# Kernel tuning notes

Hardware: AMD Instinct MI355X
Metric: run time of the kernel (lower is better)

The kernel has to match this reference:

```python
import jax, jax.numpy as jnp
import numpy as np

N, E = 50000, 800000
IN_DIM, HID, ZDIM = 256, 128, 64
LN_EPS = 1e-5


def _layernorm(x, gamma, beta):
    mu = jnp.mean(x, axis=-1, keepdims=True)
    var = jnp.mean(jnp.square(x - mu), axis=-1, keepdims=True)
    return (x - mu) * jax.lax.rsqrt(var + LN_EPS) * gamma + beta


def _gcn_conv(h, src, dst, dinv, W, b):
    # h: (N, d_in) -> (N, d_out). GCNConv: X W, then sym-normalized
    # aggregation over edges with self-loops, then bias.
    h = h @ W                                   # (N, d_out)
    coef = dinv[src] * dinv[dst]                # (E,)
    agg = jax.ops.segment_sum(h[src] * coef[:, None], dst,
                              num_segments=h.shape[0])
    agg = agg + h * jnp.square(dinv)[:, None]   # self-loop term
    return agg + b


def setup_inputs() -> dict:
    key = jax.random.key(0)
    ks = jax.random.split(key, 5)
    x = jax.random.normal(ks[0], (N, IN_DIM), dtype=jnp.float32)
    edge_index = jax.random.randint(ks[1], (2, E), 0, N, dtype=jnp.int64)
    s1 = 1.0 / np.sqrt(IN_DIM)
    s2 = 1.0 / np.sqrt(HID)
    return {
        "x": x,
        "edge_index": edge_index,
        "ln_gamma": jnp.ones((IN_DIM,), jnp.float32),
        "ln_beta": jnp.zeros((IN_DIM,), jnp.float32),
        "W1": jax.random.normal(ks[2], (IN_DIM, HID), jnp.float32) * s1,
        "b1": jnp.zeros((HID,), jnp.float32),
        "W2": jax.random.normal(ks[3], (HID, HID), jnp.float32) * s2,
        "b2": jnp.zeros((HID,), jnp.float32),
        "W3": jax.random.normal(ks[4], (HID, ZDIM), jnp.float32) * s2,
        "b3": jnp.zeros((ZDIM,), jnp.float32),
    }


def reference(x, edge_index, ln_gamma, ln_beta, W1, b1, W2, b2, W3, b3):
    src, dst = edge_index[0], edge_index[1]
    n = x.shape[0]
    # degree with self-loops (dropout is inference no-op, training=False)
    deg = jnp.ones((n,), x.dtype).at[dst].add(1.0)
    dinv = jax.lax.rsqrt(deg)
    h = _layernorm(x, ln_gamma, ln_beta)
    h = jax.nn.relu(_gcn_conv(h, src, dst, dinv, W1, b1))
    h = jax.nn.relu(_gcn_conv(h, src, dst, dinv, W2, b2))
    z = _gcn_conv(h, src, dst, dinv, W3, b3)
    return z
```

## Files before the change

kernel.cpp:

```cpp
#include <hip/hip_runtime.h>
#include <cstdint>
#include <cstddef>


typedef __attribute__((ext_vector_type(8))) __bf16 bf16x8;
typedef __attribute__((ext_vector_type(4))) float f32x4;
typedef _Float16 half_t;
typedef __attribute__((ext_vector_type(8))) _Float16 half8_t;

__global__ __launch_bounds__(256) void prep_misc(
    const float* __restrict__ x, const float* __restrict__ W1,
    const float* __restrict__ W2, const float* __restrict__ W3,
    int* __restrict__ bcnt, int* __restrict__ bcur_zero,
    unsigned short* __restrict__ W1t_hi, unsigned short* __restrict__ W1t_lo,
    unsigned short* __restrict__ W2t_hi, unsigned short* __restrict__ W2t_lo,
    unsigned short* __restrict__ W3t_hi, unsigned short* __restrict__ W3t_lo,
    float* __restrict__ mu, float* __restrict__ rs, int n) {
  int blk = blockIdx.x;
  int tid = threadIdx.x;
  if (blk == 0) {
    bcnt[tid] = 0;
    bcur_zero[tid] = 0;
    return;
  }
  if (blk <= 224) {
    int idx = (blk - 1) * 256 + tid;
    const float* W;
    unsigned short *Th, *Tl;
    int K, NOUT;
    if (idx < 32768) {
      W = W1; Th = W1t_hi; Tl = W1t_lo; K = 256; NOUT = 128;
    } else if (idx < 49152) {
      idx -= 32768;
      W = W2; Th = W2t_hi; Tl = W2t_lo; K = 128; NOUT = 128;
    } else {
      idx -= 49152;
      W = W3; Th = W3t_hi; Tl = W3t_lo; K = 128; NOUT = 64;
    }
    int k = idx / NOUT, c = idx % NOUT;
    float v = W[idx];
    __bf16 h = (__bf16)v;
    __bf16 l = (__bf16)(v - (float)h);
    Th[(size_t)c * K + k] = __builtin_bit_cast(unsigned short, h);
    Tl[(size_t)c * K + k] = __builtin_bit_cast(unsigned short, l);
    return;
  }
  int wv = (blk - 225) * 4 + (tid >> 6);
  int lane = tid & 63;
  if (wv >= n) return;
  const float4* row = (const float4*)(x + (size_t)wv * 256);
  float4 v = row[lane];
  float s = v.x + v.y + v.z + v.w;
  float s2 = v.x * v.x + v.y * v.y + v.z * v.z + v.w * v.w;
  for (int off = 32; off > 0; off >>= 1) {
    s += __shfl_down(s, off);
    s2 += __shfl_down(s2, off);
  }
  if (lane == 0) {
    float m = s * (1.0f / 256.0f);
    float var = s2 * (1.0f / 256.0f) - m * m;
    mu[wv] = m;
    rs[wv] = rsqrtf(var + 1e-5f);
  }
}

__global__ __launch_bounds__(256) void hist_bucket(const int* __restrict__ dst,
                                                   int* __restrict__ bcnt, int E, int NB) {
  __shared__ int h[256];
  int t = threadIdx.x;
  h[t] = 0;
  __syncthreads();
  for (int e = blockIdx.x * 256 + t; e < E; e += gridDim.x * 256)
    atomicAdd(&h[dst[e] >> 8], 1);
  __syncthreads();
  if (t < NB && h[t]) atomicAdd(&bcnt[t], h[t]);
}

__global__ __launch_bounds__(256) void scan_buckets(const int* __restrict__ bcnt,
                                                    int* __restrict__ bbase,
                                                    int* __restrict__ bcur, int NB, int E) {
  __shared__ int tmp[256];
  int t = threadIdx.x;
  int v = (t < NB) ? bcnt[t] : 0;
  tmp[t] = v;
  __syncthreads();
  for (int off = 1; off < 256; off <<= 1) {
    int x = (t >= off) ? tmp[t - off] : 0;
    __syncthreads();
    tmp[t] += x;
    __syncthreads();
  }
  int excl = tmp[t] - v;
  if (t < NB) { bbase[t] = excl; bcur[t] = excl; }
  if (t == 0) bbase[NB] = E;
}

#define CHUNK 4096
__global__ __launch_bounds__(256) void scatter_bins(const int* __restrict__ src,
                                                    const int* __restrict__ dst,
                                                    int* __restrict__ bcur,
                                                    int2* __restrict__ binned, int E) {
  __shared__ int2 recs[CHUNK];
  __shared__ int hist[256], lbase[256], resv[256], cur[256];
  int t = threadIdx.x;
  int e0 = blockIdx.x * CHUNK;
  if (e0 >= E) return;
  int len = min(CHUNK, E - e0);
  hist[t] = 0;
  cur[t] = 0;
  __syncthreads();
  for (int i = t; i < len; i += 256) atomicAdd(&hist[dst[e0 + i] >> 8], 1);
  __syncthreads();
  int v = hist[t];
  lbase[t] = v;
  __syncthreads();
  for (int off = 1; off < 256; off <<= 1) {
    int x = (t >= off) ? lbase[t - off] : 0;
    __syncthreads();
    lbase[t] += x;
    __syncthreads();
  }
  int myexcl = lbase[t] - v;
  if (v) resv[t] = atomicAdd(&bcur[t], v);
  __syncthreads();
  lbase[t] = myexcl;
  __syncthreads();
  for (int i = t; i < len; i += 256) {
    int d = dst[e0 + i], s = src[e0 + i];
    int b = d >> 8;
    int r = atomicAdd(&cur[b], 1);
    recs[lbase[b] + r] = make_int2(s, d);
  }
  __syncthreads();
  for (int i = t; i < len; i += 256) {
    int2 rc = recs[i];
    int b = rc.y >> 8;
    binned[resv[b] + (i - lbase[b])] = rc;
  }
}

#define MAXB 8192
__global__ __launch_bounds__(256) void sort_bucket(const int2* __restrict__ binned,
                                                   const int* __restrict__ bbase,
                                                   int* __restrict__ srcs,
                                                   int* __restrict__ offs,
                                                   float* __restrict__ dinv,
                                                   int N, int NB, int E) {
  __shared__ int2 recs[MAXB];
  __shared__ unsigned short rnk[MAXB];
  __shared__ int sstage[MAXB];
  __shared__ int hist[256], nbase[256];
  int b = blockIdx.x, t = threadIdx.x;
  int base = bbase[b], end = bbase[b + 1];
  int L = end - base;
  if (L > MAXB) L = MAXB;
  hist[t] = 0;
  __syncthreads();
  for (int i = t; i < L; i += 256) {
    int2 rc = binned[base + i];
    recs[i] = rc;
    int r = atomicAdd(&hist[rc.y & 255], 1);
    rnk[i] = (unsigned short)r;
  }
  __syncthreads();
  int v = hist[t];
  nbase[t] = v;
  __syncthreads();
  for (int off = 1; off < 256; off <<= 1) {
    int x = (t >= off) ? nbase[t - off] : 0;
    __syncthreads();
    nbase[t] += x;
    __syncthreads();
  }
  int excl = nbase[t] - v;
  __syncthreads();
  nbase[t] = excl;
  int node = (b << 8) + t;
  if (node < N) {
    offs[node] = base + excl;
    dinv[node] = rsqrtf(1.0f + (float)v);
  }
  if (b == NB - 1 && t == 0) offs[N] = E;
  __syncthreads();
  for (int i = t; i < L; i += 256) {
    int2 rc = recs[i];
    sstage[nbase[rc.y & 255] + rnk[i]] = rc.x;
  }
  __syncthreads();
  for (int i = t; i < L; i += 256) srcs[base + i] = sstage[i];
}

__global__ void fill_w(const int* __restrict__ srcs, const float* __restrict__ dinv,
                       int2* __restrict__ edges, int E) {
  int e = blockIdx.x * 256 + threadIdx.x;
  if (e < E) {
    int s = srcs[e];
    edges[e] = make_int2(s, __float_as_int(dinv[s]));
  }
}

template <int K, int NOUT, bool LN, bool A_FP16>
__launch_bounds__(256)
__global__ void gemm_mfma(const void* __restrict__ Avoid,
                          const unsigned short* __restrict__ Wt_hi,
                          const unsigned short* __restrict__ Wt_lo,
                          const float* __restrict__ mu, const float* __restrict__ rs,
                          const float* __restrict__ gamma, const float* __restrict__ beta,
                          half_t* __restrict__ out, int nrows) {
  constexpr int BM = 64, BK = 32;
  constexpr int NT = NOUT / 16;
  __shared__ unsigned short As_hi[BM][BK];
  __shared__ unsigned short As_lo[BM][BK];
  __shared__ unsigned short Bs_hi[NOUT][BK];
  __shared__ unsigned short Bs_lo[NOUT][BK];

  const int tid = threadIdx.x;
  const int lane = tid & 63;
  const int w = tid >> 6;
  const int quad = lane >> 4;
  const int l16 = lane & 15;
  const int row0 = blockIdx.x * BM;

  f32x4 acc[NT];
#pragma unroll
  for (int t = 0; t < NT; ++t) acc[t] = (f32x4){0.f, 0.f, 0.f, 0.f};

  for (int k0 = 0; k0 < K; k0 += BK) {
    if (!A_FP16) {
      const float* A = (const float*)Avoid;
#pragma unroll
      for (int i = 0; i < 2; ++i) {
        int r = i * 32 + (tid >> 3);
        int c4 = (tid & 7) * 4;
        int grow = row0 + r;
        if (grow > nrows - 1) grow = nrows - 1;
        float4 v = *(const float4*)&A[(size_t)grow * K + k0 + c4];
        if (LN) {
          float m = mu[grow], s = rs[grow];
          float4 g = *(const float4*)&gamma[k0 + c4];
          float4 b = *(const float4*)&beta[k0 + c4];
          v.x = (v.x - m) * s * g.x + b.x;
          v.y = (v.y - m) * s * g.y + b.y;
          v.z = (v.z - m) * s * g.z + b.z;
          v.w = (v.w - m) * s * g.w + b.w;
        }
        float vv[4] = {v.x, v.y, v.z, v.w};
#pragma unroll
        for (int j = 0; j < 4; ++j) {
          __bf16 h = (__bf16)vv[j];
          __bf16 l = (__bf16)(vv[j] - (float)h);
          As_hi[r][c4 + j] = __builtin_bit_cast(unsigned short, h);
          As_lo[r][c4 + j] = __builtin_bit_cast(unsigned short, l);
        }
      }
    } else {
      const half_t* A = (const half_t*)Avoid;
      int r = tid >> 2;
      int c8 = (tid & 3) * 8;
      int grow = row0 + r;
      if (grow > nrows - 1) grow = nrows - 1;
      half8_t v = *(const half8_t*)&A[(size_t)grow * K + k0 + c8];
#pragma unroll
      for (int j = 0; j < 8; ++j) {
        float f = (float)v[j];
        __bf16 h = (__bf16)f;
        __bf16 l = (__bf16)(f - (float)h);
        As_hi[r][c8 + j] = __builtin_bit_cast(unsigned short, h);
        As_lo[r][c8 + j] = __builtin_bit_cast(unsigned short, l);
      }
    }
#pragma unroll
    for (int i = 0; i < NOUT / 64; ++i) {
      int n = i * 64 + (tid >> 2);
      int c8 = (tid & 3) * 8;
      *(uint4*)&Bs_hi[n][c8] = *(const uint4*)&Wt_hi[(size_t)n * K + k0 + c8];
      *(uint4*)&Bs_lo[n][c8] = *(const uint4*)&Wt_lo[(size_t)n * K + k0 + c8];
    }
    __syncthreads();

    bf16x8 ah = *(const bf16x8*)&As_hi[w * 16 + l16][quad * 8];
    bf16x8 al = *(const bf16x8*)&As_lo[w * 16 + l16][quad * 8];
#pragma unroll
    for (int t = 0; t < NT; ++t) {
      bf16x8 bh = *(const bf16x8*)&Bs_hi[t * 16 + l16][quad * 8];
      bf16x8 bl = *(const bf16x8*)&Bs_lo[t * 16 + l16][quad * 8];
      acc[t] = __builtin_amdgcn_mfma_f32_16x16x32_bf16(ah, bh, acc[t], 0, 0, 0);
      acc[t] = __builtin_amdgcn_mfma_f32_16x16x32_bf16(al, bh, acc[t], 0, 0, 0);
      acc[t] = __builtin_amdgcn_mfma_f32_16x16x32_bf16(ah, bl, acc[t], 0, 0, 0);
    }
    __syncthreads();
  }

#pragma unroll
  for (int t = 0; t < NT; ++t) {
#pragma unroll
    for (int r = 0; r < 4; ++r) {
      int grow = row0 + w * 16 + quad * 4 + r;
      if (grow < nrows) out[(size_t)grow * NOUT + t * 16 + l16] = (half_t)acc[t][r];
    }
  }
}

__global__ __launch_bounds__(256) void agg128_h(const half_t* __restrict__ t,
                                                const int* __restrict__ offs,
                                                const int2* __restrict__ edges,
                                                const float* __restrict__ dinv,
                                                const float* __restrict__ bias,
                                                half_t* __restrict__ out, int n) {
  int gid = blockIdx.x * blockDim.x + threadIdx.x;
  int node = gid >> 6, lane = gid & 63;
  if (node >= n) return;
  int qw = lane >> 4;
  int fl = lane & 15;
  int e0 = offs[node], e1 = offs[node + 1];
  float acc[8] = {0.f, 0.f, 0.f, 0.f, 0.f, 0.f, 0.f, 0.f};
  int e = e0 + qw;
  for (; e + 12 < e1; e += 16) {
    int2 da = edges[e], db = edges[e + 4], dc = edges[e + 8], dd = edges[e + 12];
    half8_t va = *(const half8_t*)(t + ((size_t)da.x << 7) + fl * 8);
    half8_t vb = *(const half8_t*)(t + ((size_t)db.x << 7) + fl * 8);
    half8_t vc = *(const half8_t*)(t + ((size_t)dc.x << 7) + fl * 8);
    half8_t vd = *(const half8_t*)(t + ((size_t)dd.x << 7) + fl * 8);
    float wa = __int_as_float(da.y), wb = __int_as_float(db.y);
    float wc = __int_as_float(dc.y), wd = __int_as_float(dd.y);
#pragma unroll
    for (int j = 0; j < 8; ++j) {
      acc[j] = fmaf(wa, (float)va[j], acc[j]);
      acc[j] = fmaf(wb, (float)vb[j], acc[j]);
      acc[j] = fmaf(wc, (float)vc[j], acc[j]);
      acc[j] = fmaf(wd, (float)vd[j], acc[j]);
    }
  }
  for (; e < e1; e += 4) {
    int2 d = edges[e];
    half8_t v = *(const half8_t*)(t + ((size_t)d.x << 7) + fl * 8);
    float w = __int_as_float(d.y);
#pragma unroll
    for (int j = 0; j < 8; ++j) acc[j] = fmaf(w, (float)v[j], acc[j]);
  }
#pragma unroll
  for (int j = 0; j < 8; ++j) {
    acc[j] += __shfl_xor(acc[j], 16);
    acc[j] += __shfl_xor(acc[j], 32);
  }
  if (qw == 0) {
    float di = dinv[node];
    float dii = di * di;
    half8_t sv = *(const half8_t*)(t + ((size_t)node << 7) + fl * 8);
    float4 b0 = *(const float4*)(bias + fl * 8);
    float4 b1 = *(const float4*)(bias + fl * 8 + 4);
    float bb[8] = {b0.x, b0.y, b0.z, b0.w, b1.x, b1.y, b1.z, b1.w};
    half8_t o;
#pragma unroll
    for (int j = 0; j < 8; ++j) {
      float v = di * acc[j] + dii * (float)sv[j] + bb[j];
      o[j] = (half_t)fmaxf(v, 0.f);
    }
    *(half8_t*)(out + ((size_t)node << 7) + fl * 8) = o;
  }
}

__global__ __launch_bounds__(256) void agg64_h(const half_t* __restrict__ t,
                                               const int* __restrict__ offs,
                                               const int2* __restrict__ edges,
                                               const float* __restrict__ dinv,
                                               const float* __restrict__ bias,
                                               float* __restrict__ out, int n) {
  int gid = blockIdx.x * blockDim.x + threadIdx.x;
  int node = gid >> 6, lane = gid & 63;
  if (node >= n) return;
  int og = lane >> 3;
  int fl = lane & 7;
  int e0 = offs[node], e1 = offs[node + 1];
  float acc[8] = {0.f, 0.f, 0.f, 0.f, 0.f, 0.f, 0.f, 0.f};
  int e = e0 + og;
  for (; e + 8 < e1; e += 16) {
    int2 da = edges[e], db = edges[e + 8];
    half8_t va = *(const half8_t*)(t + ((size_t)da.x << 6) + fl * 8);
    half8_t vb = *(const half8_t*)(t + ((size_t)db.x << 6) + fl * 8);
    float wa = __int_as_float(da.y), wb = __int_as_float(db.y);
#pragma unroll
    for (int j = 0; j < 8; ++j) {
      acc[j] = fmaf(wa, (float)va[j], acc[j]);
      acc[j] = fmaf(wb, (float)vb[j], acc[j]);
    }
  }
  for (; e < e1; e += 8) {
    int2 d = edges[e];
    half8_t v = *(const half8_t*)(t + ((size_t)d.x << 6) + fl * 8);
    float w = __int_as_float(d.y);
#pragma unroll
    for (int j = 0; j < 8; ++j) acc[j] = fmaf(w, (float)v[j], acc[j]);
  }
#pragma unroll
  for (int j = 0; j < 8; ++j) {
    acc[j] += __shfl_xor(acc[j], 8);
    acc[j] += __shfl_xor(acc[j], 16);
    acc[j] += __shfl_xor(acc[j], 32);
  }
  if (og == 0) {
    float di = dinv[node];
    float dii = di * di;
    half8_t sv = *(const half8_t*)(t + ((size_t)node << 6) + fl * 8);
    float4 b0 = *(const float4*)(bias + fl * 8);
    float4 b1 = *(const float4*)(bias + fl * 8 + 4);
    float bb[8] = {b0.x, b0.y, b0.z, b0.w, b1.x, b1.y, b1.z, b1.w};
    float ov[8];
#pragma unroll
    for (int j = 0; j < 8; ++j) ov[j] = di * acc[j] + dii * (float)sv[j] + bb[j];
    *(float4*)(out + ((size_t)node << 6) + fl * 8) = make_float4(ov[0], ov[1], ov[2], ov[3]);
    *(float4*)(out + ((size_t)node << 6) + fl * 8 + 4) = make_float4(ov[4], ov[5], ov[6], ov[7]);
  }
}

extern "C" void kernel_launch(void* const* d_in, const int* in_sizes, int n_in,
                              void* d_out, int out_size, void* d_ws, size_t ws_size,
                              hipStream_t stream) {
  const float* x = (const float*)d_in[0];
  const int* ei = (const int*)d_in[1];
  const float* gamma = (const float*)d_in[2];
  const float* beta = (const float*)d_in[3];
  const float* W1 = (const float*)d_in[4];
  const float* b1 = (const float*)d_in[5];
  const float* W2 = (const float*)d_in[6];
  const float* b2 = (const float*)d_in[7];
  const float* W3 = (const float*)d_in[8];
  const float* b3 = (const float*)d_in[9];
  float* out = (float*)d_out;

  const int N = in_sizes[0] / 256;
  const int E = in_sizes[1] / 2;
  const int* src = ei;
  const int* dst = ei + E;
  const int NB = (N + 255) >> 8;

  char* ws = (char*)d_ws;
  auto alloc = [&](size_t bytes) -> char* {
    char* p = ws;
    ws += (bytes + 255) & ~(size_t)255;
    return p;
  };
  int* bcnt = (int*)alloc(256 * 4);
  int* bbase = (int*)alloc(257 * 4);
  int* bcur = (int*)alloc(256 * 4);
  int2* binned = (int2*)alloc((size_t)E * 8);
  int* srcs = (int*)alloc((size_t)E * 4);
  int* offs = (int*)alloc((size_t)(N + 1) * 4);
  float* dinv = (float*)alloc((size_t)N * 4);
  int2* edges = (int2*)alloc((size_t)E * 8);
  float* mu = (float*)alloc((size_t)N * 4);
  float* rs = (float*)alloc((size_t)N * 4);
  half_t* t = (half_t*)alloc((size_t)N * 128 * 2);
  half_t* h = (half_t*)alloc((size_t)N * 128 * 2);
  unsigned short* W1t_hi = (unsigned short*)alloc(256 * 128 * 2);
  unsigned short* W1t_lo = (unsigned short*)alloc(256 * 128 * 2);
  unsigned short* W2t_hi = (unsigned short*)alloc(128 * 128 * 2);
  unsigned short* W2t_lo = (unsigned short*)alloc(128 * 128 * 2);
  unsigned short* W3t_hi = (unsigned short*)alloc(128 * 64 * 2);
  unsigned short* W3t_lo = (unsigned short*)alloc(128 * 64 * 2);

  const int ln_blocks = (N + 3) / 4;
  prep_misc<<<225 + ln_blocks, 256, 0, stream>>>(
      x, W1, W2, W3, bcnt, bcur, W1t_hi, W1t_lo, W2t_hi, W2t_lo, W3t_hi, W3t_lo,
      mu, rs, N);

  hist_bucket<<<256, 256, 0, stream>>>(dst, bcnt, E, NB);
  scan_buckets<<<1, 256, 0, stream>>>(bcnt, bbase, bcur, NB, E);
  scatter_bins<<<(E + CHUNK - 1) / CHUNK, 256, 0, stream>>>(src, dst, bcur, binned, E);
  sort_bucket<<<NB, 256, 0, stream>>>(binned, bbase, srcs, offs, dinv, N, NB, E);
  fill_w<<<(E + 255) / 256, 256, 0, stream>>>(srcs, dinv, edges, E);

  const int gemm_blocks = (N + 63) / 64;
  const int agg_blocks = (N + 3) / 4;

  gemm_mfma<256, 128, true, false><<<gemm_blocks, 256, 0, stream>>>(
      x, W1t_hi, W1t_lo, mu, rs, gamma, beta, t, N);
  agg128_h<<<agg_blocks, 256, 0, stream>>>(t, offs, edges, dinv, b1, h, N);

  gemm_mfma<128, 128, false, true><<<gemm_blocks, 256, 0, stream>>>(
      h, W2t_hi, W2t_lo, nullptr, nullptr, nullptr, nullptr, t, N);
  agg128_h<<<agg_blocks, 256, 0, stream>>>(t, offs, edges, dinv, b2, h, N);

  gemm_mfma<128, 64, false, true><<<gemm_blocks, 256, 0, stream>>>(
      h, W3t_hi, W3t_lo, nullptr, nullptr, nullptr, nullptr, t, N);
  agg64_h<<<agg_blocks, 256, 0, stream>>>(t, offs, edges, dinv, b3, out, N);
}
```

Before: 291.5 us.

## Double-buffer GEMM tiles via register prefetch and pack edge records into 32 bits

The MFMA GEMM now keeps two LDS buffers and prefetches the next K tile into registers while the current tile's MFMAs run. This needs only one barrier per iteration and hides part of the global-load latency. Edge binning now packs each (dst, src) pair into one 32-bit word, which halves binned traffic. The sort pass re-reads the packed words from global memory and assigns slots with shared-memory atomics instead of staging records and ranks in LDS. The packing assumes node ids fit in 16 bits, which holds for N=50000 but not in general, and atomic slot assignment makes the per-node edge order nondeterministic.

Result: slower. 317.9 us (+9.1%).

```diff
diff --git a/kernel.cpp b/kernel.cpp
--- a/kernel.cpp
+++ b/kernel.cpp
@@ -99,8 +99,8 @@
 __global__ __launch_bounds__(256) void scatter_bins(const int* __restrict__ src,
                                                     const int* __restrict__ dst,
                                                     int* __restrict__ bcur,
-                                                    int2* __restrict__ binned, int E) {
-  __shared__ int2 recs[CHUNK];
+                                                    unsigned int* __restrict__ binned, int E) {
+  __shared__ unsigned int recs[CHUNK];
   __shared__ int hist[256], lbase[256], resv[256], cur[256];
   int t = threadIdx.x;
   int e0 = blockIdx.x * CHUNK;
@@ -129,52 +129,46 @@
     int d = dst[e0 + i], s = src[e0 + i];
     int b = d >> 8;
     int r = atomicAdd(&cur[b], 1);
-    recs[lbase[b] + r] = make_int2(s, d);
+    recs[lbase[b] + r] = ((unsigned int)d << 16) | (unsigned int)s;
   }
   __syncthreads();
   for (int i = t; i < len; i += 256) {
-    int2 rc = recs[i];
-    int b = rc.y >> 8;
+    unsigned int rc = recs[i];
+    int b = rc >> 24;
     binned[resv[b] + (i - lbase[b])] = rc;
   }
 }
 
 #define MAXB 8192
-__global__ __launch_bounds__(256) void sort_bucket(const int2* __restrict__ binned,
+__global__ __launch_bounds__(256) void sort_bucket(const unsigned int* __restrict__ binned,
                                                    const int* __restrict__ bbase,
                                                    int* __restrict__ srcs,
                                                    int* __restrict__ offs,
                                                    float* __restrict__ dinv,
                                                    int N, int NB, int E) {
-  __shared__ int2 recs[MAXB];
-  __shared__ unsigned short rnk[MAXB];
   __shared__ int sstage[MAXB];
-  __shared__ int hist[256], nbase[256];
+  __shared__ int hist[256], nbase[256], cur[256], tmp[256];
   int b = blockIdx.x, t = threadIdx.x;
   int base = bbase[b], end = bbase[b + 1];
   int L = end - base;
   if (L > MAXB) L = MAXB;
   hist[t] = 0;
   __syncthreads();
-  for (int i = t; i < L; i += 256) {
-    int2 rc = binned[base + i];
-    recs[i] = rc;
-    int r = atomicAdd(&hist[rc.y & 255], 1);
-    rnk[i] = (unsigned short)r;
-  }
+  for (int i = t; i < L; i += 256)
+    atomicAdd(&hist[(binned[base + i] >> 16) & 255], 1);
   __syncthreads();
   int v = hist[t];
-  nbase[t] = v;
+  tmp[t] = v;
   __syncthreads();
   for (int off = 1; off < 256; off <<= 1) {
-    int x = (t >= off) ? nbase[t - off] : 0;
+    int x = (t >= off) ? tmp[t - off] : 0;
     __syncthreads();
-    nbase[t] += x;
+    tmp[t] += x;
     __syncthreads();
   }
-  int excl = nbase[t] - v;
-  __syncthreads();
+  int excl = tmp[t] - v;
   nbase[t] = excl;
+  cur[t] = excl;
   int node = (b << 8) + t;
   if (node < N) {
     offs[node] = base + excl;
@@ -183,8 +177,10 @@
   if (b == NB - 1 && t == 0) offs[N] = E;
   __syncthreads();
   for (int i = t; i < L; i += 256) {
-    int2 rc = recs[i];
-    sstage[nbase[rc.y & 255] + rnk[i]] = rc.x;
+    unsigned int p = binned[base + i];
+    int ld = (p >> 16) & 255;
+    int slot = atomicAdd(&cur[ld], 1);
+    sstage[slot] = (int)(p & 0xFFFFu);
   }
   __syncthreads();
   for (int i = t; i < L; i += 256) srcs[base + i] = sstage[i];
@@ -209,10 +205,12 @@
                           half_t* __restrict__ out, int nrows) {
   constexpr int BM = 64, BK = 32;
   constexpr int NT = NOUT / 16;
-  __shared__ unsigned short As_hi[BM][BK];
-  __shared__ unsigned short As_lo[BM][BK];
-  __shared__ unsigned short Bs_hi[NOUT][BK];
-  __shared__ unsigned short Bs_lo[NOUT][BK];
+  constexpr int T = K / BK;
+  constexpr int NBI = NOUT / 64;
+  __shared__ unsigned short As_hi[2][BM][BK];
+  __shared__ unsigned short As_lo[2][BM][BK];
+  __shared__ unsigned short Bs_hi[2][NOUT][BK];
+  __shared__ unsigned short Bs_lo[2][NOUT][BK];
 
   const int tid = threadIdx.x;
   const int lane = tid & 63;
@@ -221,74 +219,104 @@
   const int l16 = lane & 15;
   const int row0 = blockIdx.x * BM;
 
-  f32x4 acc[NT];
-#pragma unroll
-  for (int t = 0; t < NT; ++t) acc[t] = (f32x4){0.f, 0.f, 0.f, 0.f};
-
-  for (int k0 = 0; k0 < K; k0 += BK) {
+  float4 a0, a1, gv, bv;
+  half8_t av;
+  uint4 bhr[NBI], blr[NBI];
+  const int rA0 = tid >> 3, c4 = (tid & 7) * 4;
+  const int rA = tid >> 2, c8a = (tid & 3) * 8;
+  const int nB = tid >> 2, c8 = (tid & 3) * 8;
+  int g0 = row0 + rA0; if (g0 > nrows - 1) g0 = nrows - 1;
+  int g1 = row0 + 32 + rA0; if (g1 > nrows - 1) g1 = nrows - 1;
+  int gA = row0 + rA; if (gA > nrows - 1) gA = nrows - 1;
+  float m0 = 0.f, s0 = 0.f, m1 = 0.f, s1 = 0.f;
+  if (LN && !A_FP16) { m0 = mu[g0]; s0 = rs[g0]; m1 = mu[g1]; s1 = rs[g1]; }
+
+  auto load_tile = [&](int k0) {
     if (!A_FP16) {
       const float* A = (const float*)Avoid;
-#pragma unroll
-      for (int i = 0; i < 2; ++i) {
-        int r = i * 32 + (tid >> 3);
-        int c4 = (tid & 7) * 4;
-        int grow = row0 + r;
-        if (grow > nrows - 1) grow = nrows - 1;
-        float4 v = *(const float4*)&A[(size_t)grow * K + k0 + c4];
-        if (LN) {
-          float m = mu[grow], s = rs[grow];
-          float4 g = *(const float4*)&gamma[k0 + c4];
-          float4 b = *(const float4*)&beta[k0 + c4];
-          v.x = (v.x - m) * s * g.x + b.x;
-          v.y = (v.y - m) * s * g.y + b.y;
-          v.z = (v.z - m) * s * g.z + b.z;
-          v.w = (v.w - m) * s * g.w + b.w;
-        }
-        float vv[4] = {v.x, v.y, v.z, v.w};
-#pragma unroll
-        for (int j = 0; j < 4; ++j) {
-          __bf16 h = (__bf16)vv[j];
-          __bf16 l = (__bf16)(vv[j] - (float)h);
-          As_hi[r][c4 + j] = __builtin_bit_cast(unsigned short, h);
-          As_lo[r][c4 + j] = __builtin_bit_cast(unsigned short, l);
-        }
+      a0 = *(const float4*)&A[(size_t)g0 * K + k0 + c4];
+      a1 = *(const float4*)&A[(size_t)g1 * K + k0 + c4];
+      if (LN) {
+        gv = *(const float4*)&gamma[k0 + c4];
+        bv = *(const float4*)&beta[k0 + c4];
       }
     } else {
       const half_t* A = (const half_t*)Avoid;
-      int r = tid >> 2;
-      int c8 = (tid & 3) * 8;
-      int grow = row0 + r;
-      if (grow > nrows - 1) grow = nrows - 1;
-      half8_t v = *(const half8_t*)&A[(size_t)grow * K + k0 + c8];
+      av = *(const half8_t*)&A[(size_t)gA * K + k0 + c8a];
+    }
+#pragma unroll
+    for (int i = 0; i < NBI; ++i) {
+      int n = i * 64 + nB;
+      bhr[i] = *(const uint4*)&Wt_hi[(size_t)n * K + k0 + c8];
+      blr[i] = *(const uint4*)&Wt_lo[(size_t)n * K + k0 + c8];
+    }
+  };
+  auto store_tile = [&](int buf) {
+    if (!A_FP16) {
+      float v0[4] = {a0.x, a0.y, a0.z, a0.w};
+      float v1[4] = {a1.x, a1.y, a1.z, a1.w};
+      if (LN) {
+        float g4[4] = {gv.x, gv.y, gv.z, gv.w};
+        float b4[4] = {bv.x, bv.y, bv.z, bv.w};
+#pragma unroll
+        for (int j = 0; j < 4; ++j) {
+          v0[j] = (v0[j] - m0) * s0 * g4[j] + b4[j];
+          v1[j] = (v1[j] - m1) * s1 * g4[j] + b4[j];
+        }
+      }
+#pragma unroll
+      for (int j = 0; j < 4; ++j) {
+        __bf16 h0 = (__bf16)v0[j];
+        As_hi[buf][rA0][c4 + j] = __builtin_bit_cast(unsigned short, h0);
+        __bf16 l0 = (__bf16)(v0[j] - (float)h0);
+        As_lo[buf][rA0][c4 + j] = __builtin_bit_cast(unsigned short, l0);
+        __bf16 h1 = (__bf16)v1[j];
+        As_hi[buf][32 + rA0][c4 + j] = __builtin_bit_cast(unsigned short, h1);
+        __bf16 l1 = (__bf16)(v1[j] - (float)h1);
+        As_lo[buf][32 + rA0][c4 + j] = __builtin_bit_cast(unsigned short, l1);
+      }
+    } else {
 #pragma unroll
       for (int j = 0; j < 8; ++j) {
-        float f = (float)v[j];
+        float f = (float)av[j];
         __bf16 h = (__bf16)f;
         __bf16 l = (__bf16)(f - (float)h);
-        As_hi[r][c8 + j] = __builtin_bit_cast(unsigned short, h);
-        As_lo[r][c8 + j] = __builtin_bit_cast(unsigned short, l);
+        As_hi[buf][rA][c8a + j] = __builtin_bit_cast(unsigned short, h);
+        As_lo[buf][rA][c8a + j] = __builtin_bit_cast(unsigned short, l);
       }
     }
 #pragma unroll
-    for (int i = 0; i < NOUT / 64; ++i) {
-      int n = i * 64 + (tid >> 2);
-      int c8 = (tid & 3) * 8;
-      *(uint4*)&Bs_hi[n][c8] = *(const uint4*)&Wt_hi[(size_t)n * K + k0 + c8];
-      *(uint4*)&Bs_lo[n][c8] = *(const uint4*)&Wt_lo[(size_t)n * K + k0 + c8];
-    }
-    __syncthreads();
-
-    bf16x8 ah = *(const bf16x8*)&As_hi[w * 16 + l16][quad * 8];
-    bf16x8 al = *(const bf16x8*)&As_lo[w * 16 + l16][quad * 8];
+    for (int i = 0; i < NBI; ++i) {
+      int n = i * 64 + nB;
+      *(uint4*)&Bs_hi[buf][n][c8] = bhr[i];
+      *(uint4*)&Bs_lo[buf][n][c8] = blr[i];
+    }
+  };
+
+  f32x4 acc[NT];
+#pragma unroll
+  for (int t = 0; t < NT; ++t) acc[t] = (f32x4){0.f, 0.f, 0.f, 0.f};
+
+  load_tile(0);
+  store_tile(0);
+  __syncthreads();
+  for (int it = 0; it < T; ++it) {
+    const int cur = it & 1;
+    if (it + 1 < T) load_tile((it + 1) * BK);
+    bf16x8 ah = *(const bf16x8*)&As_hi[cur][w * 16 + l16][quad * 8];
+    bf16x8 al = *(const bf16x8*)&As_lo[cur][w * 16 + l16][quad * 8];
 #pragma unroll
     for (int t = 0; t < NT; ++t) {
-      bf16x8 bh = *(const bf16x8*)&Bs_hi[t * 16 + l16][quad * 8];
-      bf16x8 bl = *(const bf16x8*)&Bs_lo[t * 16 + l16][quad * 8];
+      bf16x8 bh = *(const bf16x8*)&Bs_hi[cur][t * 16 + l16][quad * 8];
+      bf16x8 bl = *(const bf16x8*)&Bs_lo[cur][t * 16 + l16][quad * 8];
       acc[t] = __builtin_amdgcn_mfma_f32_16x16x32_bf16(ah, bh, acc[t], 0, 0, 0);
       acc[t] = __builtin_amdgcn_mfma_f32_16x16x32_bf16(al, bh, acc[t], 0, 0, 0);
       acc[t] = __builtin_amdgcn_mfma_f32_16x16x32_bf16(ah, bl, acc[t], 0, 0, 0);
     }
-    __syncthreads();
+    if (it + 1 < T) {
+      store_tile(1 - cur);
+      __syncthreads();
+    }
   }
 
 #pragma unroll
@@ -443,7 +471,7 @@
   int* bcnt = (int*)alloc(256 * 4);
   int* bbase = (int*)alloc(257 * 4);
   int* bcur = (int*)alloc(256 * 4);
-  int2* binned = (int2*)alloc((size_t)E * 8);
+  unsigned int* binned = (unsigned int*)alloc((size_t)E * 4);
   int* srcs = (int*)alloc((size_t)E * 4);
   int* offs = (int*)alloc((size_t)(N + 1) * 4);
   float* dinv = (float*)alloc((size_t)N * 4);
```
